# Kernel optimization log

Hardware: AMD Instinct MI355X
Metric: run time of the kernel (lower is better)

The kernel has to match this reference:

```python
import jax, jax.numpy as jnp
import numpy as np

N_NODES = 50000
HEADS = 4
OUT_DIM = 64
NEG_SLOPE = 0.2
BETA = 0.5
C_CONST = 1.0
EPS = 1e-16


def setup_inputs() -> dict:
    key = jax.random.key(0)
    ks = jax.random.split(key, 6)
    in_dim = 128
    x = jax.random.normal(ks[0], (N_NODES, in_dim), dtype=jnp.float32)
    edge_index = jax.random.randint(ks[1], (2, 800000), 0, N_NODES, dtype=jnp.int64)
    # GATConv params (glorot-ish scale)
    W = jax.random.normal(ks[2], (in_dim, HEADS * OUT_DIM), dtype=jnp.float32) * (1.0 / np.sqrt(in_dim))
    att_src = jax.random.normal(ks[3], (HEADS, OUT_DIM), dtype=jnp.float32) * (1.0 / np.sqrt(OUT_DIM))
    att_dst = jax.random.normal(ks[4], (HEADS, OUT_DIM), dtype=jnp.float32) * (1.0 / np.sqrt(OUT_DIM))
    bias = jnp.zeros((HEADS * OUT_DIM,), dtype=jnp.float32)
    return {"x": x, "edge_index": edge_index, "W": W, "att_src": att_src,
            "att_dst": att_dst, "bias": bias}


def _gat_conv(x, edge_index, W, att_src, att_dst, bias):
    N = x.shape[0]
    # add self loops (PyG GATConv default)
    loop = jnp.arange(N, dtype=edge_index.dtype)
    src = jnp.concatenate([edge_index[0], loop])
    dst = jnp.concatenate([edge_index[1], loop])
    # linear transform: [N, H, F]
    h = (x @ W).reshape(N, HEADS, OUT_DIM)
    # per-node attention logits: [N, H]
    a_src = jnp.einsum('nhf,hf->nh', h, att_src)
    a_dst = jnp.einsum('nhf,hf->nh', h, att_dst)
    # per-edge logits and segment softmax over destination nodes
    e = jax.nn.leaky_relu(a_src[src] + a_dst[dst], negative_slope=NEG_SLOPE)  # [E, H]
    m = jax.ops.segment_max(e, dst, num_segments=N)                           # [N, H]
    ex = jnp.exp(e - m[dst])
    s = jax.ops.segment_sum(ex, dst, num_segments=N)                          # [N, H]
    alpha = ex / (s[dst] + EPS)                                               # [E, H]
    # aggregate messages: [N, H, F]
    out = jax.ops.segment_sum(alpha[:, :, None] * h[src], dst, num_segments=N)
    return out.reshape(N, HEADS * OUT_DIM) + bias


def reference(x, edge_index, W, att_src, att_dst, bias):
    # eval mode: feature dropout and attention dropout are identity
    z = _gat_conv(x, edge_index, W, att_src, att_dst, bias)
    return BETA * z + (C_CONST - BETA) * jax.nn.elu(z)
```

## Files before the change

### kernel.cpp

```cpp
#include <hip/hip_runtime.h>
#include <hip/hip_bf16.h>

typedef unsigned short u16;
typedef __attribute__((ext_vector_type(8))) short bf16x8;
typedef __attribute__((ext_vector_type(4))) float f32x4;

#define HEADS 4
#define OUT_DIM 64
#define HF 256
#define IN_DIM 128
#define NEG_SLOPE 0.2f
#define EPSF 1e-16f

__device__ __forceinline__ float braw2f(u16 u) {
    union { float f; unsigned int i; } c; c.i = ((unsigned int)u) << 16; return c.f;
}
__device__ __forceinline__ u16 f2braw(float v) {
    __hip_bfloat16 t = __float2bfloat16(v);
    return *(u16*)&t;
}
__device__ __forceinline__ float lrelu(float e) { return e < 0.f ? NEG_SLOPE * e : e; }

__device__ __forceinline__ bool detect_i64(const int* ei) {
    return (ei[1] | ei[3] | ei[5] | ei[7] | ei[9] | ei[11] | ei[13] | ei[15]) == 0;
}
__device__ __forceinline__ void get_edge(const int* ei, int E, int t, bool i64,
                                         int& s, int& d) {
    if (t < E) {
        if (i64) { s = ei[2 * t]; d = ei[2 * (E + t)]; }
        else     { s = ei[t];     d = ei[E + t]; }
    } else {
        s = d = t - E;
    }
}

__global__ __launch_bounds__(256) void init_kernel(const float* __restrict__ W,
                                                   const float* __restrict__ att_s,
                                                   const float* __restrict__ att_d,
                                                   float* __restrict__ wa_s,
                                                   float* __restrict__ wa_d) {
    for (int idx = threadIdx.x; idx < HEADS * IN_DIM; idx += 256) {
        int h = idx >> 7, k = idx & 127;
        float ss = 0.f, sd = 0.f;
        for (int f = 0; f < OUT_DIM; ++f) {
            float wv = W[k * HF + h * OUT_DIM + f];
            ss = fmaf(wv, att_s[h * OUT_DIM + f], ss);
            sd = fmaf(wv, att_d[h * OUT_DIM + f], sd);
        }
        wa_s[idx] = ss;
        wa_d[idx] = sd;
    }
}

__global__ __launch_bounds__(256) void phase1_kernel(const float* __restrict__ x,
                                                     const int* __restrict__ ei,
                                                     const float* __restrict__ W,
                                                     const float* __restrict__ wa_s,
                                                     const float* __restrict__ wa_d,
                                                     float* __restrict__ a_src,
                                                     float* __restrict__ a_dst,
                                                     u16* __restrict__ xb,
                                                     u16* __restrict__ Wfrag,
                                                     int* __restrict__ cnt4,
                                                     int* __restrict__ epos,
                                                     int2* __restrict__ e2,
                                                     int N, int E, int NA, int NC) {
    int b = blockIdx.x;
    if (b < NA) {
        int wid = threadIdx.x >> 6;
        int l = threadIdx.x & 63;
        int g = l >> 4, c = l & 15, kc = c * 8;
        int v = b * 16 + wid * 4 + g;
        if (v >= N) return;

        const float4* xr = (const float4*)(x + (size_t)v * IN_DIM + kc);
        float4 x0 = xr[0], x1 = xr[1];

        uint4 u;
        u.x = (unsigned)f2braw(x0.x) | ((unsigned)f2braw(x0.y) << 16);
        u.y = (unsigned)f2braw(x0.z) | ((unsigned)f2braw(x0.w) << 16);
        u.z = (unsigned)f2braw(x1.x) | ((unsigned)f2braw(x1.y) << 16);
        u.w = (unsigned)f2braw(x1.z) | ((unsigned)f2braw(x1.w) << 16);
        *(uint4*)(xb + (size_t)v * IN_DIM + kc) = u;

        float ps[4], pd[4];
        #pragma unroll
        for (int h = 0; h < 4; ++h) {
            const float4* s4 = (const float4*)(wa_s + h * IN_DIM + kc);
            const float4* d4 = (const float4*)(wa_d + h * IN_DIM + kc);
            float4 s0 = s4[0], s1 = s4[1], d0 = d4[0], d1 = d4[1];
            ps[h] = x0.x*s0.x + x0.y*s0.y + x0.z*s0.z + x0.w*s0.w
                  + x1.x*s1.x + x1.y*s1.y + x1.z*s1.z + x1.w*s1.w;
            pd[h] = x0.x*d0.x + x0.y*d0.y + x0.z*d0.z + x0.w*d0.w
                  + x1.x*d1.x + x1.y*d1.y + x1.z*d1.z + x1.w*d1.w;
        }
        #pragma unroll
        for (int off = 1; off < 16; off <<= 1) {
            #pragma unroll
            for (int h = 0; h < 4; ++h) {
                ps[h] += __shfl_xor(ps[h], off);
                pd[h] += __shfl_xor(pd[h], off);
            }
        }
        if (c == 0) {
            float4 vs, vd;
            vs.x = ps[0]; vs.y = ps[1]; vs.z = ps[2]; vs.w = ps[3];
            vd.x = pd[0]; vd.y = pd[1]; vd.z = pd[2]; vd.w = pd[3];
            *(float4*)(a_src + (size_t)v * HEADS) = vs;
            *(float4*)(a_dst + (size_t)v * HEADS) = vd;
        }
    } else if (b < NA + NC) {
        int t = (b - NA) * 256 + threadIdx.x;
        if (t >= E + N) return;
        bool i64 = detect_i64(ei);
        int src, dst; get_edge(ei, E, t, i64, src, dst);
        bool ok = (src >= 0 && src < N && dst >= 0 && dst < N);
        int pos = 0;
        if (ok) pos = atomicAdd(cnt4 + (t & 3) * N + dst, 1);
        if (epos) {
            epos[t] = pos;
            int2 sd;
            sd.x = ok ? src : -1;
            sd.y = ok ? dst : -1;
            e2[t] = sd;
        }
    } else {
        int bb = b - NA - NC;
        for (int idx = bb * 256 + threadIdx.x; idx < 32768; idx += 8 * 256) {
            int j = idx & 7, l = (idx >> 3) & 63, t = (idx >> 9) & 3;
            int s = (idx >> 11) & 3, h = (idx >> 13) & 3;
            int k = s * 32 + ((l >> 4) & 3) * 8 + j;
            int col = h * OUT_DIM + t * 16 + (l & 15);
            Wfrag[idx] = f2braw(W[k * HF + col]);
        }
    }
}

__global__ __launch_bounds__(256) void offset_kernel(int* __restrict__ cnt4,
                                                     int* __restrict__ offs,
                                                     int* __restrict__ gcnt,
                                                     int* __restrict__ hist, int N) {
    __shared__ int lh[256];
    lh[threadIdx.x] = 0;
    __syncthreads();

    int idx = blockIdx.x * 256 + threadIdx.x;
    int l = threadIdx.x & 63;
    int d = 0;
    if (idx < N) {
        int c0 = cnt4[idx];
        int c1 = cnt4[N + idx];
        int c2 = cnt4[2 * N + idx];
        int c3 = cnt4[3 * N + idx];
        d = c0 + c1 + c2 + c3;
        cnt4[idx] = d;
        cnt4[N + idx] = c0;
        cnt4[2 * N + idx] = c0 + c1;
        cnt4[3 * N + idx] = c0 + c1 + c2;
        atomicAdd(lh + min(max(d, 0), 255), 1);
    }

    int s = d;
    #pragma unroll
    for (int off = 1; off < 64; off <<= 1) {
        int t = __shfl_up(s, off);
        if (l >= off) s += t;
    }
    int base = 0;
    if (l == 63) base = atomicAdd(gcnt, s);
    base = __shfl(base, 63);
    if (idx < N) offs[idx] = base + s - d;

    __syncthreads();
    if (lh[threadIdx.x]) atomicAdd(hist + threadIdx.x, lh[threadIdx.x]);
}

__global__ __launch_bounds__(256) void fillscatter_kernel(const int* __restrict__ ei,
                                                          const int* __restrict__ offs,
                                                          int* __restrict__ cur,
                                                          int* __restrict__ slots,
                                                          uint4* __restrict__ eslots,
                                                          const float* __restrict__ a_src,
                                                          const float* __restrict__ a_dst,
                                                          const int* __restrict__ cnt4,
                                                          const int* __restrict__ hist,
                                                          int* __restrict__ bcur,
                                                          int* __restrict__ perm,
                                                          const int* __restrict__ epos,
                                                          const int2* __restrict__ e2,
                                                          int E, int N, int NC) {
    __shared__ int sc[256];
    __shared__ int lh[256];
    __shared__ int lbase[256];

    int b = blockIdx.x;
    if (b < NC) {
        int t = b * 256 + threadIdx.x;
        if (t >= E + N) return;
        int src, dst, idx;
        if (e2) {
            int2 sd = e2[t];
            src = sd.x; dst = sd.y;
            if (src < 0) return;
            int r = t & 3;
            int base = (r == 0) ? 0 : cnt4[r * N + dst];
            idx = offs[dst] + base + epos[t];
        } else {
            bool i64 = detect_i64(ei);
            get_edge(ei, E, t, i64, src, dst);
            if (!(src >= 0 && src < N && dst >= 0 && dst < N)) return;
            int pos = atomicAdd(cur + dst, 1);
            idx = offs[dst] + pos;
        }
        if (eslots) {
            float4 as = ((const float4*)a_src)[src];
            float4 ad = ((const float4*)a_dst)[dst];
            float w0 = __expf(lrelu(as.x + ad.x));
            float w1 = __expf(lrelu(as.y + ad.y));
            float w2 = __expf(lrelu(as.z + ad.z));
            float w3 = __expf(lrelu(as.w + ad.w));
            uint4 rec;
            rec.x = (unsigned)src;
            rec.y = (unsigned)f2braw(w0) | ((unsigned)f2braw(w1) << 16);
            rec.z = (unsigned)f2braw(w2) | ((unsigned)f2braw(w3) << 16);
            rec.w = 0;
            eslots[idx] = rec;
        } else {
            slots[idx] = src;
        }
    } else {
        int tid = threadIdx.x;
        sc[tid] = hist[tid];
        lh[tid] = 0;
        __syncthreads();
        #pragma unroll
        for (int off = 1; off < 256; off <<= 1) {
            int tv = (tid >= off) ? sc[tid - off] : 0;
            __syncthreads();
            sc[tid] += tv;
            __syncthreads();
        }

        int idx = (b - NC) * 256 + tid;
        int bk = 0, mypos = 0;
        bool valid = (idx < N);
        if (valid) {
            bk = min(max(cnt4[idx], 0), 255);
            mypos = atomicAdd(lh + bk, 1);
        }
        __syncthreads();
        int c = lh[tid];
        if (c) lbase[tid] = atomicAdd(bcur + tid, c);
        __syncthreads();
        if (valid) {
            int p = (N - sc[bk]) + lbase[bk] + mypos;
            if (p >= 0 && p < N) perm[p] = idx;
        }
    }
}

#define ACC_EDGE(w01, w23, r) do { \
    float w0_ = braw2f((w01) & 0xffff), w1_ = braw2f((w01) >> 16); \
    float w2_ = braw2f((w23) & 0xffff), w3_ = braw2f((w23) >> 16); \
    ls0 += w0_; ls1 += w1_; ls2 += w2_; ls3 += w3_; \
    float xv_[8]; \
    xv_[0] = braw2f((r).x & 0xffff); xv_[1] = braw2f((r).x >> 16); \
    xv_[2] = braw2f((r).y & 0xffff); xv_[3] = braw2f((r).y >> 16); \
    xv_[4] = braw2f((r).z & 0xffff); xv_[5] = braw2f((r).z >> 16); \
    xv_[6] = braw2f((r).w & 0xffff); xv_[7] = braw2f((r).w >> 16); \
    _Pragma("unroll") \
    for (int q_ = 0; q_ < 8; ++q_) { \
        G0[q_] = fmaf(w0_, xv_[q_], G0[q_]); \
        G1[q_] = fmaf(w1_, xv_[q_], G1[q_]); \
        G2[q_] = fmaf(w2_, xv_[q_], G2[q_]); \
        G3[q_] = fmaf(w3_, xv_[q_], G3[q_]); \
    } \
} while (0)

__global__ __launch_bounds__(512) void fused_gz_kernel(const int* __restrict__ perm,
                                                       const int* __restrict__ offs,
                                                       const int* __restrict__ cnt,
                                                       const uint4* __restrict__ eslots,
                                                       const u16* __restrict__ xb,
                                                       const u16* __restrict__ Wfrag,
                                                       const float* __restrict__ bias,
                                                       float* __restrict__ out,
                                                       int N, int ET) {
    __shared__ u16 smem[32 * 520];
    __shared__ int pvals[32];

    int tid = threadIdx.x;
    int wid = tid >> 6;
    int l = tid & 63;
    int g = l >> 4, c = l & 15, kc = c * 8;
    int n = wid * 4 + g;
    int pidx = blockIdx.x * 32 + n;

    int v = -1;
    if (pidx < N) {
        v = perm[pidx];
        if (v < 0 || v >= N) v = -1;
    }
    if (c == 0) pvals[n] = v;

    int beg = 0, end = 0;
    if (v >= 0) {
        beg = offs[v];
        int deg = cnt[v];
        beg = max(0, min(beg, ET));
        end = max(beg, min(beg + deg, ET));
    }

    float ls0 = 0.f, ls1 = 0.f, ls2 = 0.f, ls3 = 0.f;
    float G0[8] = {0,0,0,0,0,0,0,0};
    float G1[8] = {0,0,0,0,0,0,0,0};
    float G2[8] = {0,0,0,0,0,0,0,0};
    float G3[8] = {0,0,0,0,0,0,0,0};

    int j = beg;
    for (; j + 4 <= end; j += 4) {
        uint4 m0 = eslots[j];
        uint4 m1 = eslots[j + 1];
        uint4 m2 = eslots[j + 2];
        uint4 m3 = eslots[j + 3];
        int s0 = max(0, min((int)m0.x, N - 1));
        int s1 = max(0, min((int)m1.x, N - 1));
        int s2 = max(0, min((int)m2.x, N - 1));
        int s3 = max(0, min((int)m3.x, N - 1));
        uint4 r0 = *(const uint4*)(xb + (size_t)s0 * IN_DIM + kc);
        uint4 r1 = *(const uint4*)(xb + (size_t)s1 * IN_DIM + kc);
        uint4 r2 = *(const uint4*)(xb + (size_t)s2 * IN_DIM + kc);
        uint4 r3 = *(const uint4*)(xb + (size_t)s3 * IN_DIM + kc);
        ACC_EDGE(m0.y, m0.z, r0);
        ACC_EDGE(m1.y, m1.z, r1);
        ACC_EDGE(m2.y, m2.z, r2);
        ACC_EDGE(m3.y, m3.z, r3);
    }
    for (; j < end; ++j) {
        uint4 m0 = eslots[j];
        int s0 = max(0, min((int)m0.x, N - 1));
        uint4 r0 = *(const uint4*)(xb + (size_t)s0 * IN_DIM + kc);
        ACC_EDGE(m0.y, m0.z, r0);
    }

    if (v >= 0) {
        float i0 = 1.f / (ls0 + EPSF), i1 = 1.f / (ls1 + EPSF);
        float i2 = 1.f / (ls2 + EPSF), i3 = 1.f / (ls3 + EPSF);
        u16* lp = smem + n * 520 + c * 8;
        #pragma unroll
        for (int h = 0; h < 4; ++h) {
            const float* G = h == 0 ? G0 : h == 1 ? G1 : h == 2 ? G2 : G3;
            float inv = h == 0 ? i0 : h == 1 ? i1 : h == 2 ? i2 : i3;
            uint4 u;
            u.x = (unsigned)f2braw(G[0] * inv) | ((unsigned)f2braw(G[1] * inv) << 16);
            u.y = (unsigned)f2braw(G[2] * inv) | ((unsigned)f2braw(G[3] * inv) << 16);
            u.z = (unsigned)f2braw(G[4] * inv) | ((unsigned)f2braw(G[5] * inv) << 16);
            u.w = (unsigned)f2braw(G[6] * inv) | ((unsigned)f2braw(G[7] * inv) << 16);
            *(uint4*)(lp + h * 128) = u;
        }
    } else {
        u16* lp = smem + n * 520 + c * 8;
        uint4 z = {0, 0, 0, 0};
        #pragma unroll
        for (int h = 0; h < 4; ++h) *(uint4*)(lp + h * 128) = z;
    }
    __syncthreads();

    int t = wid >> 2;
    int h = wid & 3;
    int q = l >> 4, mcol = l & 15;

    const u16* lp = smem + (t * 16 + mcol) * 520 + h * 128 + q * 8;
    bf16x8 A[4];
    A[0] = *(const bf16x8*)(lp);
    A[1] = *(const bf16x8*)(lp + 32);
    A[2] = *(const bf16x8*)(lp + 64);
    A[3] = *(const bf16x8*)(lp + 96);

    f32x4 acc0 = {0.f,0.f,0.f,0.f}, acc1 = acc0, acc2 = acc0, acc3 = acc0;
    #pragma unroll
    for (int s = 0; s < 4; ++s) {
        const u16* wb = Wfrag + (((h * 4 + s) * 4) << 9) + l * 8;
        bf16x8 B0 = *(const bf16x8*)(wb);
        bf16x8 B1 = *(const bf16x8*)(wb + 512);
        bf16x8 B2 = *(const bf16x8*)(wb + 1024);
        bf16x8 B3 = *(const bf16x8*)(wb + 1536);
        acc0 = __builtin_amdgcn_mfma_f32_16x16x32_bf16(A[s], B0, acc0, 0, 0, 0);
        acc1 = __builtin_amdgcn_mfma_f32_16x16x32_bf16(A[s], B1, acc1, 0, 0, 0);
        acc2 = __builtin_amdgcn_mfma_f32_16x16x32_bf16(A[s], B2, acc2, 0, 0, 0);
        acc3 = __builtin_amdgcn_mfma_f32_16x16x32_bf16(A[s], B3, acc3, 0, 0, 0);
    }

    #pragma unroll
    for (int bt = 0; bt < 4; ++bt) {
        f32x4 a = bt == 0 ? acc0 : bt == 1 ? acc1 : bt == 2 ? acc2 : acc3;
        float b = bias[h * OUT_DIM + bt * 16 + mcol];
        #pragma unroll
        for (int r = 0; r < 4; ++r) {
            int vv = pvals[t * 16 + q * 4 + r];
            if (vv >= 0) {
                float z = a[r] + b;
                float y = z > 0.f ? z : 0.5f * z + 0.5f * (__expf(z) - 1.f);
                out[(size_t)vv * HF + h * OUT_DIM + bt * 16 + mcol] = y;
            }
        }
    }
}

__global__ __launch_bounds__(512) void gather_bf_kernel(const int* __restrict__ offs,
                                                        const int* __restrict__ cnt,
                                                        const int* __restrict__ slots,
                                                        const u16* __restrict__ xb,
                                                        const float* __restrict__ a_src,
                                                        const float* __restrict__ a_dst,
                                                        u16* __restrict__ Gout, int N, int ET) {
    int v = (blockIdx.x * 512 + threadIdx.x) >> 6;
    int l = threadIdx.x & 63;
    if (v >= N) return;
    int h = l >> 4, c = l & 15, kc = c * 8;

    int beg = offs[v];
    int deg = cnt[v];
    beg = max(0, min(beg, ET));
    int end = max(beg, min(beg + deg, ET));
    float adh = a_dst[v * HEADS + h];

    float ls = 0.f;
    float G[8] = {0.f,0.f,0.f,0.f,0.f,0.f,0.f,0.f};

    int j = beg;
    for (; j + 4 <= end; j += 4) {
        int s0 = max(0, min(slots[j],     N - 1));
        int s1 = max(0, min(slots[j + 1], N - 1));
        int s2 = max(0, min(slots[j + 2], N - 1));
        int s3 = max(0, min(slots[j + 3], N - 1));
        float w0 = __expf(lrelu(a_src[s0 * HEADS + h] + adh));
        float w1 = __expf(lrelu(a_src[s1 * HEADS + h] + adh));
        float w2 = __expf(lrelu(a_src[s2 * HEADS + h] + adh));
        float w3 = __expf(lrelu(a_src[s3 * HEADS + h] + adh));
        uint4 r0 = *(const uint4*)(xb + (size_t)s0 * IN_DIM + kc);
        uint4 r1 = *(const uint4*)(xb + (size_t)s1 * IN_DIM + kc);
        uint4 r2 = *(const uint4*)(xb + (size_t)s2 * IN_DIM + kc);
        uint4 r3 = *(const uint4*)(xb + (size_t)s3 * IN_DIM + kc);
        ls += (w0 + w1) + (w2 + w3);
        unsigned ua[4];
        ua[0]=r0.x; ua[1]=r0.y; ua[2]=r0.z; ua[3]=r0.w;
        #pragma unroll
        for (int q = 0; q < 4; ++q) {
            G[2*q]   = fmaf(w0, braw2f(ua[q] & 0xffff), G[2*q]);
            G[2*q+1] = fmaf(w0, braw2f(ua[q] >> 16),    G[2*q+1]);
        }
        ua[0]=r1.x; ua[1]=r1.y; ua[2]=r1.z; ua[3]=r1.w;
        #pragma unroll
        for (int q = 0; q < 4; ++q) {
            G[2*q]   = fmaf(w1, braw2f(ua[q] & 0xffff), G[2*q]);
            G[2*q+1] = fmaf(w1, braw2f(ua[q] >> 16),    G[2*q+1]);
        }
        ua[0]=r2.x; ua[1]=r2.y; ua[2]=r2.z; ua[3]=r2.w;
        #pragma unroll
        for (int q = 0; q < 4; ++q) {
            G[2*q]   = fmaf(w2, braw2f(ua[q] & 0xffff), G[2*q]);
            G[2*q+1] = fmaf(w2, braw2f(ua[q] >> 16),    G[2*q+1]);
        }
        ua[0]=r3.x; ua[1]=r3.y; ua[2]=r3.z; ua[3]=r3.w;
        #pragma unroll
        for (int q = 0; q < 4; ++q) {
            G[2*q]   = fmaf(w3, braw2f(ua[q] & 0xffff), G[2*q]);
            G[2*q+1] = fmaf(w3, braw2f(ua[q] >> 16),    G[2*q+1]);
        }
    }
    for (; j < end; ++j) {
        int s0 = max(0, min(slots[j], N - 1));
        float w0 = __expf(lrelu(a_src[s0 * HEADS + h] + adh));
        uint4 r0 = *(const uint4*)(xb + (size_t)s0 * IN_DIM + kc);
        ls += w0;
        unsigned ua[4]; ua[0]=r0.x; ua[1]=r0.y; ua[2]=r0.z; ua[3]=r0.w;
        #pragma unroll
        for (int q = 0; q < 4; ++q) {
            G[2*q]   = fmaf(w0, braw2f(ua[q] & 0xffff), G[2*q]);
            G[2*q+1] = fmaf(w0, braw2f(ua[q] >> 16),    G[2*q+1]);
        }
    }

    float inv = 1.f / (ls + EPSF);
    uint4 u;
    u.x = (unsigned)f2braw(G[0] * inv) | ((unsigned)f2braw(G[1] * inv) << 16);
    u.y = (unsigned)f2braw(G[2] * inv) | ((unsigned)f2braw(G[3] * inv) << 16);
    u.z = (unsigned)f2braw(G[4] * inv) | ((unsigned)f2braw(G[5] * inv) << 16);
    u.w = (unsigned)f2braw(G[6] * inv) | ((unsigned)f2braw(G[7] * inv) << 16);
    *(uint4*)(Gout + (size_t)v * 512 + h * 128 + kc) = u;
}

__global__ __launch_bounds__(512) void gather_f32_kernel(const int* __restrict__ offs,
                                                         const int* __restrict__ cnt,
                                                         const int* __restrict__ slots,
                                                         const float* __restrict__ x,
                                                         const float* __restrict__ a_src,
                                                         const float* __restrict__ a_dst,
                                                         u16* __restrict__ Gout, int N, int ET) {
    int v = (blockIdx.x * 512 + threadIdx.x) >> 6;
    int l = threadIdx.x & 63;
    if (v >= N) return;
    int h = l >> 4, c = l & 15, kc = c * 8;

    int beg = offs[v];
    int deg = cnt[v];
    beg = max(0, min(beg, ET));
    int end = max(beg, min(beg + deg, ET));
    float adh = a_dst[v * HEADS + h];

    float ls = 0.f;
    float G[8] = {0.f,0.f,0.f,0.f,0.f,0.f,0.f,0.f};
    for (int j = beg; j < end; ++j) {
        int s0 = max(0, min(slots[j], N - 1));
        float w0 = __expf(lrelu(a_src[s0 * HEADS + h] + adh));
        const float4* xr0 = (const float4*)(x + (size_t)s0 * IN_DIM + kc);
        float4 a0 = xr0[0], b0 = xr0[1];
        ls += w0;
        G[0]=fmaf(w0,a0.x,G[0]); G[1]=fmaf(w0,a0.y,G[1]);
        G[2]=fmaf(w0,a0.z,G[2]); G[3]=fmaf(w0,a0.w,G[3]);
        G[4]=fmaf(w0,b0.x,G[4]); G[5]=fmaf(w0,b0.y,G[5]);
        G[6]=fmaf(w0,b0.z,G[6]); G[7]=fmaf(w0,b0.w,G[7]);
    }
    float inv = 1.f / (ls + EPSF);
    uint4 u;
    u.x = (unsigned)f2braw(G[0] * inv) | ((unsigned)f2braw(G[1] * inv) << 16);
    u.y = (unsigned)f2braw(G[2] * inv) | ((unsigned)f2braw(G[3] * inv) << 16);
    u.z = (unsigned)f2braw(G[4] * inv) | ((unsigned)f2braw(G[5] * inv) << 16);
    u.w = (unsigned)f2braw(G[6] * inv) | ((unsigned)f2braw(G[7] * inv) << 16);
    *(uint4*)(Gout + (size_t)v * 512 + h * 128 + kc) = u;
}

__global__ __launch_bounds__(256) void zgemm_kernel(const u16* __restrict__ Wfrag,
                                                    const float* __restrict__ bias,
                                                    float* __restrict__ out, int N) {
    int h = threadIdx.x >> 6;
    int l = threadIdx.x & 63;
    int q = l >> 4, mcol = l & 15;
    int nb = blockIdx.x * 16;

    const u16* G = (const u16*)out;
    bool valid = (nb + mcol) < N;
    int vA = valid ? nb + mcol : N - 1;
    const u16* gp = G + (size_t)vA * 512 + h * 128 + q * 8;
    bf16x8 A[4];
    A[0] = *(const bf16x8*)(gp);
    A[1] = *(const bf16x8*)(gp + 32);
    A[2] = *(const bf16x8*)(gp + 64);
    A[3] = *(const bf16x8*)(gp + 96);
    if (!valid) {
        bf16x8 zz = {0,0,0,0,0,0,0,0};
        A[0] = zz; A[1] = zz; A[2] = zz; A[3] = zz;
    }

    f32x4 acc0 = {0.f,0.f,0.f,0.f}, acc1 = acc0, acc2 = acc0, acc3 = acc0;
    #pragma unroll
    for (int s = 0; s < 4; ++s) {
        const u16* wb = Wfrag + (((h * 4 + s) * 4) << 9) + l * 8;
        bf16x8 B0 = *(const bf16x8*)(wb);
        bf16x8 B1 = *(const bf16x8*)(wb + 512);
        bf16x8 B2 = *(const bf16x8*)(wb + 1024);
        bf16x8 B3 = *(const bf16x8*)(wb + 1536);
        acc0 = __builtin_amdgcn_mfma_f32_16x16x32_bf16(A[s], B0, acc0, 0, 0, 0);
        acc1 = __builtin_amdgcn_mfma_f32_16x16x32_bf16(A[s], B1, acc1, 0, 0, 0);
        acc2 = __builtin_amdgcn_mfma_f32_16x16x32_bf16(A[s], B2, acc2, 0, 0, 0);
        acc3 = __builtin_amdgcn_mfma_f32_16x16x32_bf16(A[s], B3, acc3, 0, 0, 0);
    }

    #pragma unroll
    for (int t = 0; t < 4; ++t) {
        f32x4 a = t == 0 ? acc0 : t == 1 ? acc1 : t == 2 ? acc2 : acc3;
        float b = bias[h * OUT_DIM + t * 16 + mcol];
        #pragma unroll
        for (int r = 0; r < 4; ++r) {
            int v = nb + q * 4 + r;
            if (v < N) {
                float z = a[r] + b;
                float y = z > 0.f ? z : 0.5f * z + 0.5f * (__expf(z) - 1.f);
                out[(size_t)v * HF + h * OUT_DIM + t * 16 + mcol] = y;
            }
        }
    }
}

extern "C" void kernel_launch(void* const* d_in, const int* in_sizes, int n_in,
                              void* d_out, int out_size, void* d_ws, size_t ws_size,
                              hipStream_t stream) {
    const float* x       = (const float*)d_in[0];
    const int*   ei      = (const int*)d_in[1];
    const float* W       = (const float*)d_in[2];
    const float* att_src = (const float*)d_in[3];
    const float* att_dst = (const float*)d_in[4];
    const float* bias    = (const float*)d_in[5];

    const int N = in_sizes[0] / IN_DIM;
    const int E = in_sizes[1] / 2;
    const int ET = E + N;
    const int NT = (N + 255) / 256;

    char* ws = (char*)d_ws;
    size_t off = 0;
    float* wa_s   = (float*)(ws + off); off += HEADS * IN_DIM * 4;
    float* wa_d   = (float*)(ws + off); off += HEADS * IN_DIM * 4;
    u16*   Wfrag  = (u16*)(ws + off);   off += 32768 * 2;
    float* a_src  = (float*)(ws + off); off += (size_t)N * HEADS * 4;
    float* a_dst  = (float*)(ws + off); off += (size_t)N * HEADS * 4;
    int*   offs   = (int*)(ws + off);   off += ((size_t)N * 4 + 15) & ~(size_t)15;
    size_t zero_beg = off;
    int*   cnt4   = (int*)(ws + off);   off += ((size_t)N * 16 + 15) & ~(size_t)15;
    int*   cur    = (int*)(ws + off);   off += ((size_t)N * 4 + 15) & ~(size_t)15;
    int*   gcnt   = (int*)(ws + off);   off += 64;
    int*   hist   = (int*)(ws + off);   off += 256 * 4;
    int*   bcur   = (int*)(ws + off);   off += 256 * 4;
    size_t zero_end = off;
    int*   perm   = (int*)(ws + off);   off += ((size_t)N * 4 + 15) & ~(size_t)15;
    int*   slots  = (int*)(ws + off);   off += ((size_t)ET * 4 + 15) & ~(size_t)15;
    u16*   xb     = (u16*)(ws + off);   size_t need_bf = off + (size_t)N * IN_DIM * 2;
    uint4* eslots = (uint4*)(ws + need_bf);
    size_t need_w = need_bf + (size_t)ET * 16;
    int*   epos   = (int*)(ws + need_w);
    int2*  e2     = (int2*)(ws + need_w + (((size_t)ET * 4 + 15) & ~(size_t)15));
    size_t need_pos = need_w + (((size_t)ET * 4 + 15) & ~(size_t)15)
                             + (size_t)ET * 8;
    bool use_bf  = (ws_size >= need_bf);
    bool use_w   = (ws_size >= need_w);
    bool use_pos = (ws_size >= need_pos) && use_w;

    const int NA = (N + 15) / 16;
    const int NC = (ET + 255) / 256;

    hipMemsetAsync(ws + zero_beg, 0, zero_end - zero_beg, stream);
    init_kernel<<<1, 256, 0, stream>>>(W, att_src, att_dst, wa_s, wa_d);
    phase1_kernel<<<NA + NC + 8, 256, 0, stream>>>(x, ei, W, wa_s, wa_d, a_src, a_dst,
                                                   use_bf ? xb : (u16*)d_out,
                                                   Wfrag, cnt4,
                                                   use_pos ? epos : (int*)0,
                                                   use_pos ? e2 : (int2*)0,
                                                   N, E, NA, NC);
    offset_kernel<<<NT, 256, 0, stream>>>(cnt4, offs, gcnt, hist, N);
    fillscatter_kernel<<<NC + (use_w ? NT : 0), 256, 0, stream>>>(
        ei, offs, cur, slots, use_w ? eslots : (uint4*)0, a_src, a_dst,
        cnt4, hist, bcur, perm,
        use_pos ? epos : (int*)0, use_pos ? e2 : (int2*)0,
        E, N, NC);
    if (use_w) {
        fused_gz_kernel<<<(N + 31) / 32, 512, 0, stream>>>(perm, offs, cnt4, eslots,
                                                           xb, Wfrag, bias,
                                                           (float*)d_out, N, ET);
    } else if (use_bf) {
        gather_bf_kernel<<<(N * 64 + 511) / 512, 512, 0, stream>>>(offs, cnt4, slots, xb,
                                                                   a_src, a_dst,
                                                                   (u16*)d_out, N, ET);
        zgemm_kernel<<<(N + 15) / 16, 256, 0, stream>>>(Wfrag, bias, (float*)d_out, N);
    } else {
        gather_f32_kernel<<<(N * 64 + 511) / 512, 512, 0, stream>>>(offs, cnt4, slots, x,
                                                                    a_src, a_dst,
                                                                    (u16*)d_out, N, ET);
        zgemm_kernel<<<(N + 15) / 16, 256, 0, stream>>>(Wfrag, bias, (float*)d_out, N);
    }
}
```

Baseline: 236.4 us.

## Handle self-loops analytically in aggregation and pack edge info into one record

Self-loop edges are no longer materialized through counting, scattering and slot storage. Each destination's own contribution is added directly in the gather kernels from a_src/a_dst and its own feature row. The per-edge position and src/dst arrays are merged into one 16-byte record written and read with nontemporal stores and loads, and the eslots writes are also nontemporal. This cuts atomics, scatter traffic and edge records by N per call, but changes the slot layout, since offsets no longer include self-loops, so every consumer has to stay consistent.

```diff
diff --git a/kernel.cpp b/kernel.cpp
--- a/kernel.cpp
+++ b/kernel.cpp
@@ -4,6 +4,7 @@
 typedef unsigned short u16;
 typedef __attribute__((ext_vector_type(8))) short bf16x8;
 typedef __attribute__((ext_vector_type(4))) float f32x4;
+typedef __attribute__((ext_vector_type(4))) int i32x4;
 
 #define HEADS 4
 #define OUT_DIM 64
@@ -23,15 +24,6 @@
 
 __device__ __forceinline__ bool detect_i64(const int* ei) {
     return (ei[1] | ei[3] | ei[5] | ei[7] | ei[9] | ei[11] | ei[13] | ei[15]) == 0;
-}
-__device__ __forceinline__ void get_edge(const int* ei, int E, int t, bool i64,
-                                         int& s, int& d) {
-    if (t < E) {
-        if (i64) { s = ei[2 * t]; d = ei[2 * (E + t)]; }
-        else     { s = ei[t];     d = ei[E + t]; }
-    } else {
-        s = d = t - E;
-    }
 }
 
 __global__ __launch_bounds__(256) void init_kernel(const float* __restrict__ W,
@@ -62,8 +54,7 @@
                                                      u16* __restrict__ xb,
                                                      u16* __restrict__ Wfrag,
                                                      int* __restrict__ cnt4,
-                                                     int* __restrict__ epos,
-                                                     int2* __restrict__ e2,
+                                                     int* __restrict__ einfo,
                                                      int N, int E, int NA, int NC) {
     int b = blockIdx.x;
     if (b < NA) {
@@ -111,18 +102,21 @@
         }
     } else if (b < NA + NC) {
         int t = (b - NA) * 256 + threadIdx.x;
-        if (t >= E + N) return;
+        if (t >= E) return;
         bool i64 = detect_i64(ei);
-        int src, dst; get_edge(ei, E, t, i64, src, dst);
+        int src, dst;
+        if (i64) { src = ei[2 * t]; dst = ei[2 * (E + t)]; }
+        else     { src = ei[t];     dst = ei[E + t]; }
         bool ok = (src >= 0 && src < N && dst >= 0 && dst < N);
         int pos = 0;
         if (ok) pos = atomicAdd(cnt4 + (t & 3) * N + dst, 1);
-        if (epos) {
-            epos[t] = pos;
-            int2 sd;
-            sd.x = ok ? src : -1;
-            sd.y = ok ? dst : -1;
-            e2[t] = sd;
+        if (einfo) {
+            i32x4 rec;
+            rec.x = ok ? src : -1;
+            rec.y = ok ? dst : 0;
+            rec.z = pos;
+            rec.w = 0;
+            __builtin_nontemporal_store(rec, (i32x4*)(einfo + 4 * (size_t)t));
         }
     } else {
         int bb = b - NA - NC;
@@ -179,15 +173,14 @@
                                                           const int* __restrict__ offs,
                                                           int* __restrict__ cur,
                                                           int* __restrict__ slots,
-                                                          uint4* __restrict__ eslots,
+                                                          unsigned* __restrict__ eslots,
                                                           const float* __restrict__ a_src,
                                                           const float* __restrict__ a_dst,
                                                           const int* __restrict__ cnt4,
                                                           const int* __restrict__ hist,
                                                           int* __restrict__ bcur,
                                                           int* __restrict__ perm,
-                                                          const int* __restrict__ epos,
-                                                          const int2* __restrict__ e2,
+                                                          const int* __restrict__ einfo,
                                                           int E, int N, int NC) {
     __shared__ int sc[256];
     __shared__ int lh[256];
@@ -196,18 +189,19 @@
     int b = blockIdx.x;
     if (b < NC) {
         int t = b * 256 + threadIdx.x;
-        if (t >= E + N) return;
+        if (t >= E) return;
         int src, dst, idx;
-        if (e2) {
-            int2 sd = e2[t];
-            src = sd.x; dst = sd.y;
+        if (einfo) {
+            i32x4 rec = __builtin_nontemporal_load((const i32x4*)(einfo + 4 * (size_t)t));
+            src = rec.x; dst = rec.y;
             if (src < 0) return;
             int r = t & 3;
             int base = (r == 0) ? 0 : cnt4[r * N + dst];
-            idx = offs[dst] + base + epos[t];
+            idx = offs[dst] + base + rec.z;
         } else {
             bool i64 = detect_i64(ei);
-            get_edge(ei, E, t, i64, src, dst);
+            if (i64) { src = ei[2 * t]; dst = ei[2 * (E + t)]; }
+            else     { src = ei[t];     dst = ei[E + t]; }
             if (!(src >= 0 && src < N && dst >= 0 && dst < N)) return;
             int pos = atomicAdd(cur + dst, 1);
             idx = offs[dst] + pos;
@@ -219,12 +213,12 @@
             float w1 = __expf(lrelu(as.y + ad.y));
             float w2 = __expf(lrelu(as.z + ad.z));
             float w3 = __expf(lrelu(as.w + ad.w));
-            uint4 rec;
-            rec.x = (unsigned)src;
-            rec.y = (unsigned)f2braw(w0) | ((unsigned)f2braw(w1) << 16);
-            rec.z = (unsigned)f2braw(w2) | ((unsigned)f2braw(w3) << 16);
+            i32x4 rec;
+            rec.x = src;
+            rec.y = (int)((unsigned)f2braw(w0) | ((unsigned)f2braw(w1) << 16));
+            rec.z = (int)((unsigned)f2braw(w2) | ((unsigned)f2braw(w3) << 16));
             rec.w = 0;
-            eslots[idx] = rec;
+            __builtin_nontemporal_store(rec, (i32x4*)(eslots + 4 * (size_t)idx));
         } else {
             slots[idx] = src;
         }
@@ -260,8 +254,8 @@
 }
 
 #define ACC_EDGE(w01, w23, r) do { \
-    float w0_ = braw2f((w01) & 0xffff), w1_ = braw2f((w01) >> 16); \
-    float w2_ = braw2f((w23) & 0xffff), w3_ = braw2f((w23) >> 16); \
+    float w0_ = braw2f((w01) & 0xffff), w1_ = braw2f((unsigned)(w01) >> 16); \
+    float w2_ = braw2f((w23) & 0xffff), w3_ = braw2f((unsigned)(w23) >> 16); \
     ls0 += w0_; ls1 += w1_; ls2 += w2_; ls3 += w3_; \
     float xv_[8]; \
     xv_[0] = braw2f((r).x & 0xffff); xv_[1] = braw2f((r).x >> 16); \
@@ -277,12 +271,30 @@
     } \
 } while (0)
 
+#define ACC_EDGE_F(w0_, w1_, w2_, w3_, r) do { \
+    ls0 += w0_; ls1 += w1_; ls2 += w2_; ls3 += w3_; \
+    float xv_[8]; \
+    xv_[0] = braw2f((r).x & 0xffff); xv_[1] = braw2f((r).x >> 16); \
+    xv_[2] = braw2f((r).y & 0xffff); xv_[3] = braw2f((r).y >> 16); \
+    xv_[4] = braw2f((r).z & 0xffff); xv_[5] = braw2f((r).z >> 16); \
+    xv_[6] = braw2f((r).w & 0xffff); xv_[7] = braw2f((r).w >> 16); \
+    _Pragma("unroll") \
+    for (int q_ = 0; q_ < 8; ++q_) { \
+        G0[q_] = fmaf(w0_, xv_[q_], G0[q_]); \
+        G1[q_] = fmaf(w1_, xv_[q_], G1[q_]); \
+        G2[q_] = fmaf(w2_, xv_[q_], G2[q_]); \
+        G3[q_] = fmaf(w3_, xv_[q_], G3[q_]); \
+    } \
+} while (0)
+
 __global__ __launch_bounds__(512) void fused_gz_kernel(const int* __restrict__ perm,
                                                        const int* __restrict__ offs,
                                                        const int* __restrict__ cnt,
                                                        const uint4* __restrict__ eslots,
                                                        const u16* __restrict__ xb,
                                                        const u16* __restrict__ Wfrag,
+                                                       const float* __restrict__ a_src,
+                                                       const float* __restrict__ a_dst,
                                                        const float* __restrict__ bias,
                                                        float* __restrict__ out,
                                                        int N, int ET) {
@@ -303,19 +315,28 @@
     }
     if (c == 0) pvals[n] = v;
 
+    float ls0 = 0.f, ls1 = 0.f, ls2 = 0.f, ls3 = 0.f;
+    float G0[8] = {0,0,0,0,0,0,0,0};
+    float G1[8] = {0,0,0,0,0,0,0,0};
+    float G2[8] = {0,0,0,0,0,0,0,0};
+    float G3[8] = {0,0,0,0,0,0,0,0};
+
     int beg = 0, end = 0;
     if (v >= 0) {
         beg = offs[v];
         int deg = cnt[v];
         beg = max(0, min(beg, ET));
         end = max(beg, min(beg + deg, ET));
-    }
-
-    float ls0 = 0.f, ls1 = 0.f, ls2 = 0.f, ls3 = 0.f;
-    float G0[8] = {0,0,0,0,0,0,0,0};
-    float G1[8] = {0,0,0,0,0,0,0,0};
-    float G2[8] = {0,0,0,0,0,0,0,0};
-    float G3[8] = {0,0,0,0,0,0,0,0};
+
+        float4 as = ((const float4*)a_src)[v];
+        float4 ad = ((const float4*)a_dst)[v];
+        float sw0 = __expf(lrelu(as.x + ad.x));
+        float sw1 = __expf(lrelu(as.y + ad.y));
+        float sw2 = __expf(lrelu(as.z + ad.z));
+        float sw3 = __expf(lrelu(as.w + ad.w));
+        uint4 rs = *(const uint4*)(xb + (size_t)v * IN_DIM + kc);
+        ACC_EDGE_F(sw0, sw1, sw2, sw3, rs);
+    }
 
     int j = beg;
     for (; j + 4 <= end; j += 4) {
@@ -428,6 +449,18 @@
     float ls = 0.f;
     float G[8] = {0.f,0.f,0.f,0.f,0.f,0.f,0.f,0.f};
 
+    {
+        float w0 = __expf(lrelu(a_src[v * HEADS + h] + adh));
+        uint4 r0 = *(const uint4*)(xb + (size_t)v * IN_DIM + kc);
+        ls += w0;
+        unsigned ua[4]; ua[0]=r0.x; ua[1]=r0.y; ua[2]=r0.z; ua[3]=r0.w;
+        #pragma unroll
+        for (int q = 0; q < 4; ++q) {
+            G[2*q]   = fmaf(w0, braw2f(ua[q] & 0xffff), G[2*q]);
+            G[2*q+1] = fmaf(w0, braw2f(ua[q] >> 16),    G[2*q+1]);
+        }
+    }
+
     int j = beg;
     for (; j + 4 <= end; j += 4) {
         int s0 = max(0, min(slots[j],     N - 1));
@@ -511,6 +544,18 @@
 
     float ls = 0.f;
     float G[8] = {0.f,0.f,0.f,0.f,0.f,0.f,0.f,0.f};
+
+    {
+        float w0 = __expf(lrelu(a_src[v * HEADS + h] + adh));
+        const float4* xr0 = (const float4*)(x + (size_t)v * IN_DIM + kc);
+        float4 a0 = xr0[0], b0 = xr0[1];
+        ls += w0;
+        G[0]=fmaf(w0,a0.x,G[0]); G[1]=fmaf(w0,a0.y,G[1]);
+        G[2]=fmaf(w0,a0.z,G[2]); G[3]=fmaf(w0,a0.w,G[3]);
+        G[4]=fmaf(w0,b0.x,G[4]); G[5]=fmaf(w0,b0.y,G[5]);
+        G[6]=fmaf(w0,b0.z,G[6]); G[7]=fmaf(w0,b0.w,G[7]);
+    }
+
     for (int j = beg; j < end; ++j) {
         int s0 = max(0, min(slots[j], N - 1));
         float w0 = __expf(lrelu(a_src[s0 * HEADS + h] + adh));
@@ -616,37 +661,35 @@
     int*   perm   = (int*)(ws + off);   off += ((size_t)N * 4 + 15) & ~(size_t)15;
     int*   slots  = (int*)(ws + off);   off += ((size_t)ET * 4 + 15) & ~(size_t)15;
     u16*   xb     = (u16*)(ws + off);   size_t need_bf = off + (size_t)N * IN_DIM * 2;
-    uint4* eslots = (uint4*)(ws + need_bf);
+    unsigned* eslots = (unsigned*)(ws + need_bf);
     size_t need_w = need_bf + (size_t)ET * 16;
-    int*   epos   = (int*)(ws + need_w);
-    int2*  e2     = (int2*)(ws + need_w + (((size_t)ET * 4 + 15) & ~(size_t)15));
-    size_t need_pos = need_w + (((size_t)ET * 4 + 15) & ~(size_t)15)
-                             + (size_t)ET * 8;
+    int*   einfo  = (int*)(ws + need_w);
+    size_t need_pos = need_w + (size_t)E * 16;
     bool use_bf  = (ws_size >= need_bf);
     bool use_w   = (ws_size >= need_w);
     bool use_pos = (ws_size >= need_pos) && use_w;
 
     const int NA = (N + 15) / 16;
-    const int NC = (ET + 255) / 256;
+    const int NC = (E + 255) / 256;
 
     hipMemsetAsync(ws + zero_beg, 0, zero_end - zero_beg, stream);
     init_kernel<<<1, 256, 0, stream>>>(W, att_src, att_dst, wa_s, wa_d);
     phase1_kernel<<<NA + NC + 8, 256, 0, stream>>>(x, ei, W, wa_s, wa_d, a_src, a_dst,
                                                    use_bf ? xb : (u16*)d_out,
                                                    Wfrag, cnt4,
-                                                   use_pos ? epos : (int*)0,
-                                                   use_pos ? e2 : (int2*)0,
+                                                   use_pos ? einfo : (int*)0,
                                                    N, E, NA, NC);
     offset_kernel<<<NT, 256, 0, stream>>>(cnt4, offs, gcnt, hist, N);
     fillscatter_kernel<<<NC + (use_w ? NT : 0), 256, 0, stream>>>(
-        ei, offs, cur, slots, use_w ? eslots : (uint4*)0, a_src, a_dst,
+        ei, offs, cur, slots, use_w ? eslots : (unsigned*)0, a_src, a_dst,
         cnt4, hist, bcur, perm,
-        use_pos ? epos : (int*)0, use_pos ? e2 : (int2*)0,
+        use_pos ? einfo : (int*)0,
         E, N, NC);
     if (use_w) {
-        fused_gz_kernel<<<(N + 31) / 32, 512, 0, stream>>>(perm, offs, cnt4, eslots,
-                                                           xb, Wfrag, bias,
-                                                           (float*)d_out, N, ET);
+        fused_gz_kernel<<<(N + 31) / 32, 512, 0, stream>>>(perm, offs, cnt4,
+                                                           (const uint4*)eslots,
+                                                           xb, Wfrag, a_src, a_dst,
+                                                           bias, (float*)d_out, N, ET);
     } else if (use_bf) {
         gather_bf_kernel<<<(N * 64 + 511) / 512, 512, 0, stream>>>(offs, cnt4, slots, xb,
                                                                    a_src, a_dst,
```

New measurement: 252.1 us. 6.6% more time.
